# Optimization experiments

Hardware: AMD Instinct MI355X
Metric: run time of the kernel (lower is better)

## Reference

```python
import jax, jax.numpy as jnp
import numpy as np

BS, NS, NSTEP = 128, 1024, 8
IN_DIM, HID, MLP = 768, 512, 512
NEG = -100000.0


def setup_inputs() -> dict:
    key = jax.random.key(0)
    ks = jax.random.split(key, 12)
    s_h = 1.0 / np.sqrt(HID)
    s_cat = 1.0 / np.sqrt(HID + IN_DIM)
    s_m = 1.0 / np.sqrt(MLP)
    # gumbel noise implements Categorical sampling as argmax(logits + gumbel)
    u = jax.random.uniform(ks[9], (NSTEP, BS, NS), jnp.float32, 1e-7, 1.0 - 1e-7)
    return {
        "target_emb": jax.random.normal(ks[0], (BS, IN_DIM), jnp.float32),
        "ctx_emb": jax.random.normal(ks[1], (BS, NS, IN_DIM), jnp.float32),
        "target_len": jax.random.randint(ks[2], (BS,), 1, 32),
        "ctx_len": jax.random.randint(ks[3], (BS,), NSTEP, NS + 1),
        "n_step": NSTEP,
        "W_ih": jax.random.normal(ks[4], (4 * HID, IN_DIM), jnp.float32) * s_h,
        "W_hh": jax.random.normal(ks[5], (4 * HID, HID), jnp.float32) * s_h,
        "b_ih": jnp.zeros((4 * HID,), jnp.float32),
        "b_hh": jnp.zeros((4 * HID,), jnp.float32),
        "W1c": jax.random.normal(ks[6], (MLP, IN_DIM), jnp.float32) * s_cat,
        "W1h": jax.random.normal(ks[7], (MLP, HID), jnp.float32) * s_cat,
        "b1": jnp.zeros((MLP,), jnp.float32),
        "w2": jax.random.normal(ks[8], (MLP,), jnp.float32) * s_m,
        "b2": jnp.zeros((), jnp.float32),
        "gumbel": -jnp.log(-jnp.log(u)),
    }


def reference(target_emb, ctx_emb, target_len, ctx_len, n_step,
              W_ih, W_hh, b_ih, b_hh, W1c, W1h, b1, w2, b2, gumbel):
    bs, ns, in_dim = ctx_emb.shape
    hid = W_hh.shape[1]
    # mlp1 split: ctx part is constant across steps (concat([ctx, h]) @ W1^T = ctx@W1c^T + h@W1h^T)
    ctx_part = jnp.einsum('bnd,md->bnm', ctx_emb, W1c) + b1  # [bs, ns, mlp]
    mask0 = jnp.where(jnp.arange(ns)[None, :] >= ctx_len[:, None], NEG, 0.0).astype(jnp.float32)
    h0 = jnp.zeros((bs, hid), jnp.float32)
    c0 = jnp.zeros((bs, hid), jnp.float32)
    lp0 = jnp.zeros((bs,), jnp.float32)
    batch_idx = jnp.arange(bs)

    def step(carry, g):
        h, c, mask, x, lp = carry
        # LSTMCell (torch gate order: i, f, g, o); dropout is identity (eval semantics)
        gates = x @ W_ih.T + b_ih + h @ W_hh.T + b_hh
        i_g, f_g, g_g, o_g = jnp.split(gates, 4, axis=-1)
        c_new = jax.nn.sigmoid(f_g) * c + jax.nn.sigmoid(i_g) * jnp.tanh(g_g)
        h_new = jax.nn.sigmoid(o_g) * jnp.tanh(c_new)
        # attention-style MLP score
        pre = ctx_part + (h_new @ W1h.T)[:, None, :]          # [bs, ns, mlp]
        sc = jnp.tanh(pre) @ w2 + b2 + mask                   # [bs, ns]
        # Categorical(probs=softmax(sc)).sample() via Gumbel-argmax
        out = jnp.argmax(sc + g, axis=-1)                     # [bs]
        lp = lp + jnp.take_along_axis(jax.nn.log_softmax(sc, axis=-1), out[:, None], 1)[:, 0]
        mask = mask.at[batch_idx, out].set(NEG)
        x_new = jnp.take_along_axis(ctx_emb, out[:, None, None], axis=1)[:, 0, :]
        return (h_new, c_new, mask, x_new, lp), out

    (h, c, mask, x, log_probs), outputs = jax.lax.scan(
        step, (h0, c0, mask0, target_emb, lp0), gumbel)
    return outputs, log_probs
```

## Files before the change

kernel.cpp:

```cpp
#include <hip/hip_runtime.h>
#include <hip/hip_bf16.h>

#define BSZ 128
#define NSQ 1024
#define NSTEPC 8
#define IND 768
#define HIDD 512
#define G4D 2048
#define MLPD 512
#define KXD 1280
#define NEGV -100000.0f
#define KSG 16
#define KSH 8
#define MSPLIT 4

typedef __attribute__((ext_vector_type(4))) float f32x4;
typedef __attribute__((ext_vector_type(8))) short short8v;

__device__ __forceinline__ float bf2f(unsigned short u) {
  unsigned int x = ((unsigned int)u) << 16;
  return __builtin_bit_cast(float, x);
}

__device__ __forceinline__ float tanh_fast(float x) {
  x = fminf(fmaxf(x, -15.0f), 15.0f);
  float e = __builtin_amdgcn_exp2f(x * 2.8853900817779268f);
  float r = __builtin_amdgcn_rcpf(e + 1.0f);
  return fmaf(-2.0f, r, 1.0f);
}

__global__ __launch_bounds__(256) void k_init(
    const float* __restrict__ te, const int* __restrict__ cl,
    float* __restrict__ mask, float* __restrict__ xh,
    float* __restrict__ cst, float* __restrict__ lp) {
  const int b = blockIdx.x, tid = threadIdx.x;
  const int L = cl[b];
  for (int n = tid; n < NSQ; n += 256) mask[(size_t)b*NSQ + n] = (n >= L) ? NEGV : 0.0f;
  for (int d = tid; d < IND; d += 256) xh[(size_t)b*KXD + d] = te[(size_t)b*IND + d];
  for (int j = tid; j < HIDD; j += 256) {
    xh[(size_t)b*KXD + IND + j] = 0.0f;
    cst[(size_t)b*HIDD + j] = 0.0f;
  }
  if (tid == 0) lp[b] = 0.0f;
}

__global__ __launch_bounds__(256) void k_ctx_mfma(
    const float* __restrict__ A,
    const float* __restrict__ W,
    const float* __restrict__ bias,
    const int* __restrict__ clen,
    float* __restrict__ cp) {
  __shared__ short sCh[128*32], sCl[128*32], sWh[128*32], sWl[128*32];
  __shared__ float sb1[128];
  const int m0 = blockIdx.x * 128;
  const int i0 = blockIdx.y * 128;
  const int b = i0 >> 10;
  const int nbase = i0 & 1023;
  if (nbase >= clen[b]) return;
  const int tid = threadIdx.x;
  if (tid < 128) sb1[tid] = bias[m0 + tid];
  const int lane = tid & 63;
  const int wid = tid >> 6;
  const int wm = wid & 1, wn = wid >> 1;
  const int l15 = lane & 15, l4 = lane >> 4;

  f32x4 acc[4][4] = {};

  for (int k0 = 0; k0 < IND; k0 += 32) {
#pragma unroll
    for (int u = 0; u < 2; ++u) {
      const int c = tid + u * 256;
      const int row = c >> 2, kcs = c & 3;
      const int kread = kcs ^ ((row >> 1) & 3);
      const int off = row * 32 + kcs * 8;
      {
        const float* s = W + (size_t)(m0 + row) * IND + k0 + kread * 8;
        const float4 f0 = *(const float4*)s, f1 = *(const float4*)(s + 4);
        const float fv[8] = {f0.x, f0.y, f0.z, f0.w, f1.x, f1.y, f1.z, f1.w};
        short8v hi, lo;
#pragma unroll
        for (int j = 0; j < 8; ++j) {
          const unsigned int ub = __builtin_bit_cast(unsigned int, fv[j]);
          const unsigned int hb = ub & 0xFFFF0000u;
          const float lf = fv[j] - __builtin_bit_cast(float, hb);
          hi[j] = (short)(hb >> 16);
          lo[j] = (short)(__builtin_bit_cast(unsigned int, lf) >> 16);
        }
        *(short8v*)&sWh[off] = hi;
        *(short8v*)&sWl[off] = lo;
      }
      {
        const float* s = A + (size_t)(i0 + row) * IND + k0 + kread * 8;
        const float4 f0 = *(const float4*)s, f1 = *(const float4*)(s + 4);
        const float fv[8] = {f0.x, f0.y, f0.z, f0.w, f1.x, f1.y, f1.z, f1.w};
        short8v hi, lo;
#pragma unroll
        for (int j = 0; j < 8; ++j) {
          const unsigned int ub = __builtin_bit_cast(unsigned int, fv[j]);
          const unsigned int hb = ub & 0xFFFF0000u;
          const float lf = fv[j] - __builtin_bit_cast(float, hb);
          hi[j] = (short)(hb >> 16);
          lo[j] = (short)(__builtin_bit_cast(unsigned int, lf) >> 16);
        }
        *(short8v*)&sCh[off] = hi;
        *(short8v*)&sCl[off] = lo;
      }
    }
    __syncthreads();
    short8v wh[4], wl[4], chv[4], clv[4];
#pragma unroll
    for (int f = 0; f < 4; ++f) {
      const int rw = wm * 64 + f * 16 + l15;
      const int offw = rw * 32 + ((l4 ^ ((rw >> 1) & 3)) << 3);
      wh[f] = *(const short8v*)&sWh[offw];
      wl[f] = *(const short8v*)&sWl[offw];
      const int rc = wn * 64 + f * 16 + l15;
      const int offc = rc * 32 + ((l4 ^ ((rc >> 1) & 3)) << 3);
      chv[f] = *(const short8v*)&sCh[offc];
      clv[f] = *(const short8v*)&sCl[offc];
    }
#pragma unroll
    for (int fm = 0; fm < 4; ++fm)
#pragma unroll
      for (int fn = 0; fn < 4; ++fn) {
        acc[fm][fn] = __builtin_amdgcn_mfma_f32_16x16x32_bf16(wh[fm], chv[fn], acc[fm][fn], 0, 0, 0);
        acc[fm][fn] = __builtin_amdgcn_mfma_f32_16x16x32_bf16(wh[fm], clv[fn], acc[fm][fn], 0, 0, 0);
        acc[fm][fn] = __builtin_amdgcn_mfma_f32_16x16x32_bf16(wl[fm], chv[fn], acc[fm][fn], 0, 0, 0);
      }
    __syncthreads();
  }
#pragma unroll
  for (int fm = 0; fm < 4; ++fm) {
#pragma unroll
    for (int r = 0; r < 4; ++r) {
      const int m = m0 + wm * 64 + fm * 16 + l4 * 4 + r;
      const float bb = sb1[m - m0];
      float* dst = cp + (((size_t)(b * MLPD + m)) << 10) + nbase + wn * 64 + l15;
#pragma unroll
      for (int fn = 0; fn < 4; ++fn)
        dst[fn * 16] = acc[fm][fn][r] + bb;
    }
  }
}

__global__ __launch_bounds__(256) void k_pgemm(
    const float* __restrict__ A, int lda, int acol,
    const float* __restrict__ B0, int ldb0, int kb,
    const float* __restrict__ B1, int ldb1,
    int kTiles, int N, float* __restrict__ P) {
  __shared__ float As[16][128];
  __shared__ float Bs[16][132];
  const int n0 = blockIdx.x * 128;
  const int kc0 = blockIdx.y * kTiles * 16;
  const int tid = threadIdx.x;
  const int tn = tid & 15;
  const int ta = tid >> 4;
  float acc[8][8] = {};
  for (int t = 0; t < kTiles; ++t) {
    const int k0 = kc0 + t * 16;
#pragma unroll
    for (int u = 0; u < 2; ++u) {
      const int v = tid + u * 256;
      const int r = v >> 2, kc = v & 3;
      const float4 a4 = *(const float4*)(A + (size_t)r * lda + acol + k0 + kc * 4);
      As[kc*4+0][r] = a4.x; As[kc*4+1][r] = a4.y; As[kc*4+2][r] = a4.z; As[kc*4+3][r] = a4.w;
      const float* bp = (k0 < kb) ? (B0 + (size_t)(n0 + r) * ldb0 + k0 + kc * 4)
                                  : (B1 + (size_t)(n0 + r) * ldb1 + (k0 - kb) + kc * 4);
      const float4 b4 = *(const float4*)bp;
      Bs[kc*4+0][r] = b4.x; Bs[kc*4+1][r] = b4.y; Bs[kc*4+2][r] = b4.z; Bs[kc*4+3][r] = b4.w;
    }
    __syncthreads();
#pragma unroll
    for (int kk = 0; kk < 16; ++kk) {
      float av[8], bv[8];
#pragma unroll
      for (int q = 0; q < 8; ++q) av[q] = As[kk][ta*8+q];
#pragma unroll
      for (int q = 0; q < 8; ++q) bv[q] = Bs[kk][tn*8+q];
#pragma unroll
      for (int ri = 0; ri < 8; ++ri)
#pragma unroll
        for (int ni = 0; ni < 8; ++ni)
          acc[ri][ni] = fmaf(av[ri], bv[ni], acc[ri][ni]);
    }
    __syncthreads();
  }
#pragma unroll
  for (int ri = 0; ri < 8; ++ri) {
    const int i = ta * 8 + ri;
    float* p = P + ((size_t)blockIdx.y * BSZ + i) * N + n0 + tn * 8;
    *(float4*)(p + 0) = make_float4(acc[ri][0], acc[ri][1], acc[ri][2], acc[ri][3]);
    *(float4*)(p + 4) = make_float4(acc[ri][4], acc[ri][5], acc[ri][6], acc[ri][7]);
  }
}

__global__ __launch_bounds__(512) void k_lstm(
    const float* __restrict__ gp, const float* __restrict__ b_ih,
    const float* __restrict__ b_hh, float* __restrict__ cst, float* __restrict__ xh) {
  const int b = blockIdx.x, j = threadIdx.x;
  float g[4];
#pragma unroll
  for (int q = 0; q < 4; ++q) {
    float s = b_ih[q*HIDD + j] + b_hh[q*HIDD + j];
#pragma unroll
    for (int ks = 0; ks < KSG; ++ks) s += gp[((size_t)ks*BSZ + b)*G4D + q*HIDD + j];
    g[q] = s;
  }
  const float c_old = cst[(size_t)b*HIDD + j];
  const float ig = 1.0f / (1.0f + expf(-g[0]));
  const float fg = 1.0f / (1.0f + expf(-g[1]));
  const float gg = tanhf(g[2]);
  const float og = 1.0f / (1.0f + expf(-g[3]));
  const float cn = fg * c_old + ig * gg;
  const float hn = og * tanhf(cn);
  cst[(size_t)b*HIDD + j] = cn;
  xh[(size_t)b*KXD + IND + j] = hn;
}

__global__ __launch_bounds__(256) void k_scores(
    const float* __restrict__ cp, const float* __restrict__ hpp,
    const float* __restrict__ w2, const int* __restrict__ clen,
    float* __restrict__ psc) {
  const int mh = blockIdx.x;
  const int b = blockIdx.y;
  const int tid = threadIdx.x;
  __shared__ float hs[128], ws[128];
  if (tid < 128) {
    const int m = mh * 128 + tid;
    float s = 0.0f;
#pragma unroll
    for (int ks = 0; ks < KSH; ++ks) s += hpp[((size_t)ks*BSZ + b)*MLPD + m];
    hs[tid] = s;
    ws[tid] = w2[m];
  }
  __syncthreads();
  const int len = clen[b];
  const int n0 = tid * 4;
  if (n0 >= len) return;
  float ax = 0, ay = 0, az = 0, aw = 0;
  const float* base = cp + ((size_t)b * MLPD + mh * 128) * NSQ + n0;
#pragma unroll 4
  for (int mm = 0; mm < 128; ++mm) {
    const float4 c4 = *(const float4*)(base + (size_t)mm * NSQ);
    const float h = hs[mm], w = ws[mm];
    ax = fmaf(tanh_fast(c4.x + h), w, ax);
    ay = fmaf(tanh_fast(c4.y + h), w, ay);
    az = fmaf(tanh_fast(c4.z + h), w, az);
    aw = fmaf(tanh_fast(c4.w + h), w, aw);
  }
  *(float4*)(psc + ((size_t)b * MSPLIT + mh) * NSQ + n0) = make_float4(ax, ay, az, aw);
}

__global__ __launch_bounds__(256) void k_argmax(
    const float* __restrict__ psc, float* __restrict__ mask,
    const float* __restrict__ gum, const float* __restrict__ b2p,
    float* __restrict__ lp, const float* __restrict__ ctx,
    float* __restrict__ xh, float* __restrict__ outv, int step) {
  const int b = blockIdx.x, tid = threadIdx.x;
  __shared__ float rv[256], rs[256], rm[256];
  __shared__ int ri[256];
  __shared__ int sel;
  const float b2 = b2p[0];
  const int n0 = tid * 4;
  const float4 m4 = *(const float4*)(mask + (size_t)b * NSQ + n0);
  float sc[4] = {b2 + m4.x, b2 + m4.y, b2 + m4.z, b2 + m4.w};
#pragma unroll
  for (int mh = 0; mh < MSPLIT; ++mh) {
    const float4 p4 = *(const float4*)(psc + ((size_t)b * MSPLIT + mh) * NSQ + n0);
    sc[0] += p4.x; sc[1] += p4.y; sc[2] += p4.z; sc[3] += p4.w;
  }
  const float4 g4 = *(const float4*)(gum + ((size_t)step * BSZ + b) * NSQ + n0);
  const float gv[4] = {g4.x, g4.y, g4.z, g4.w};
  float bestv = -1e30f, bests = 0.0f, msc = -1e30f;
  int bestn = 0;
#pragma unroll
  for (int q = 0; q < 4; ++q) {
    const float v = sc[q] + gv[q];
    if (v > bestv) { bestv = v; bestn = n0 + q; bests = sc[q]; }
    msc = fmaxf(msc, sc[q]);
  }
  rv[tid] = bestv; ri[tid] = bestn; rs[tid] = bests; rm[tid] = msc;
  __syncthreads();
  for (int o = 128; o > 0; o >>= 1) {
    if (tid < o) {
      if (rv[tid+o] > rv[tid] || (rv[tid+o] == rv[tid] && ri[tid+o] < ri[tid])) {
        rv[tid] = rv[tid+o]; ri[tid] = ri[tid+o]; rs[tid] = rs[tid+o];
      }
      rm[tid] = fmaxf(rm[tid], rm[tid+o]);
    }
    __syncthreads();
  }
  const float M = rm[0];
  __syncthreads();
  float se = 0.0f;
#pragma unroll
  for (int q = 0; q < 4; ++q)
    se += __builtin_amdgcn_exp2f((sc[q] - M) * 1.4426950408889634f);
  rm[tid] = se;
  __syncthreads();
  for (int o = 128; o > 0; o >>= 1) {
    if (tid < o) rm[tid] += rm[tid+o];
    __syncthreads();
  }
  if (tid == 0) {
    const int n = ri[0];
    const float lse = M + logf(rm[0]);
    const float nlp = lp[b] + rs[0] - lse;
    lp[b] = nlp;
    mask[(size_t)b * NSQ + n] = NEGV;
    outv[step * BSZ + b] = (float)n;
    if (step == NSTEPC - 1) outv[NSTEPC * BSZ + b] = nlp;
    sel = n;
  }
  __syncthreads();
  const int n = sel;
  const float4* src = (const float4*)(ctx + ((size_t)b * NSQ + n) * IND);
  float4* dst = (float4*)(xh + (size_t)b * KXD);
  for (int d = tid; d < IND / 4; d += 256) dst[d] = src[d];
}

extern "C" void kernel_launch(void* const* d_in, const int* in_sizes, int n_in,
                              void* d_out, int out_size, void* d_ws, size_t ws_size,
                              hipStream_t stream) {
  const float* target_emb = (const float*)d_in[0];
  const float* ctx_emb   = (const float*)d_in[1];
  const int*   ctx_len   = (const int*)d_in[3];
  const float* W_ih = (const float*)d_in[5];
  const float* W_hh = (const float*)d_in[6];
  const float* b_ih = (const float*)d_in[7];
  const float* b_hh = (const float*)d_in[8];
  const float* W1c  = (const float*)d_in[9];
  const float* W1h  = (const float*)d_in[10];
  const float* b1   = (const float*)d_in[11];
  const float* w2   = (const float*)d_in[12];
  const float* b2   = (const float*)d_in[13];
  const float* gumbel = (const float*)d_in[14];
  float* out = (float*)d_out;

  float* ws = (float*)d_ws;
  size_t off = 0;
  auto alloc = [&](size_t n) { float* p = ws + off; off += (n + 63) & ~(size_t)63; return p; };

  float* cp   = alloc((size_t)BSZ * MLPD * NSQ);
  float* gp   = alloc((size_t)KSG * BSZ * G4D);
  float* hpp  = alloc((size_t)KSH * BSZ * MLPD);
  float* psc  = alloc((size_t)BSZ * MSPLIT * NSQ);
  float* mask = alloc((size_t)BSZ * NSQ);
  float* xh   = alloc((size_t)BSZ * KXD);
  float* cst  = alloc((size_t)BSZ * HIDD);
  float* lp   = alloc(128);

  k_init<<<BSZ, 256, 0, stream>>>(target_emb, ctx_len, mask, xh, cst, lp);

  k_ctx_mfma<<<dim3(MLPD/128, (BSZ*NSQ)/128), 256, 0, stream>>>(
      ctx_emb, W1c, b1, ctx_len, cp);

  for (int t = 0; t < NSTEPC; ++t) {
    k_pgemm<<<dim3(G4D/128, KSG), 256, 0, stream>>>(
        xh, KXD, 0, W_ih, IND, IND, W_hh, HIDD, 5, G4D, gp);
    k_lstm<<<BSZ, 512, 0, stream>>>(gp, b_ih, b_hh, cst, xh);
    k_pgemm<<<dim3(MLPD/128, KSH), 256, 0, stream>>>(
        xh, KXD, IND, W1h, HIDD, 1 << 30, nullptr, 0, 4, MLPD, hpp);
    k_scores<<<dim3(MSPLIT, BSZ), 256, 0, stream>>>(cp, hpp, w2, ctx_len, psc);
    k_argmax<<<BSZ, 256, 0, stream>>>(psc, mask, gumbel, b2, lp, ctx_emb, xh, out, t);
  }
}
```

Measured before the change: 909.2 us.

## Pre-split W1c to bf16 hi/lo and double-buffer the ctx GEMM with async LDS loads

Adds a prep kernel that splits W1c once into swizzled bf16 hi/lo tiles, so the context GEMM no longer re-splits the weight in every block. The new ctx kernel streams the weight tiles directly into LDS with global_load_lds and double-buffers both operands, prefetching the next K tile while the MFMAs run on the current one. Block indices are remapped so that blocks sharing ctx rows run close together, which should improve cache reuse. In exchange it adds an extra launch, extra workspace, and a larger LDS footprint from the doubled buffers, which may lower occupancy.

Result: faster. 857.7 us (-5.7%).

```diff
diff --git a/kernel.cpp b/kernel.cpp
--- a/kernel.cpp
+++ b/kernel.cpp
@@ -17,9 +17,22 @@
 typedef __attribute__((ext_vector_type(4))) float f32x4;
 typedef __attribute__((ext_vector_type(8))) short short8v;
 
-__device__ __forceinline__ float bf2f(unsigned short u) {
-  unsigned int x = ((unsigned int)u) << 16;
-  return __builtin_bit_cast(float, x);
+__device__ __forceinline__ void gl16(const unsigned short* g, unsigned short* l) {
+  __builtin_amdgcn_global_load_lds(
+      (const __attribute__((address_space(1))) unsigned int*)(g),
+      (__attribute__((address_space(3))) unsigned int*)(l), 16, 0, 0);
+}
+
+__device__ __forceinline__ void split2(float4 f0, float4 f1, short8v& hi, short8v& lo) {
+  float fv[8] = {f0.x, f0.y, f0.z, f0.w, f1.x, f1.y, f1.z, f1.w};
+#pragma unroll
+  for (int j = 0; j < 8; ++j) {
+    const unsigned ub = __builtin_bit_cast(unsigned, fv[j]);
+    const unsigned hb = ub & 0xFFFF0000u;
+    const float lf = fv[j] - __builtin_bit_cast(float, hb);
+    hi[j] = (short)(hb >> 16);
+    lo[j] = (short)(__builtin_bit_cast(unsigned, lf) >> 16);
+  }
 }
 
 __device__ __forceinline__ float tanh_fast(float x) {
@@ -27,6 +40,23 @@
   float e = __builtin_amdgcn_exp2f(x * 2.8853900817779268f);
   float r = __builtin_amdgcn_rcpf(e + 1.0f);
   return fmaf(-2.0f, r, 1.0f);
+}
+
+__global__ __launch_bounds__(256) void k_prep_w1c(
+    const float* __restrict__ W1c,
+    unsigned short* __restrict__ wch, unsigned short* __restrict__ wcl) {
+  const int c = blockIdx.x * 256 + threadIdx.x;
+  if (c >= 49152) return;
+  const int row = c / 96, wc = c - row * 96;
+  const int tile = wc >> 2, c4 = wc & 3;
+  const int slot = c4 ^ ((row >> 1) & 3);
+  const size_t unit = ((size_t)((row >> 7) * 24 + tile) * 128 + (row & 127)) * 4 + slot;
+  const float* src = W1c + (size_t)row * IND + wc * 8;
+  const float4 f0 = *(const float4*)src, f1 = *(const float4*)(src + 4);
+  short8v hi, lo;
+  split2(f0, f1, hi, lo);
+  *(short8v*)(wch + unit * 8) = hi;
+  *(short8v*)(wcl + unit * 8) = lo;
 }
 
 __global__ __launch_bounds__(256) void k_init(
@@ -44,89 +74,99 @@
   if (tid == 0) lp[b] = 0.0f;
 }
 
-__global__ __launch_bounds__(256) void k_ctx_mfma(
-    const float* __restrict__ A,
-    const float* __restrict__ W,
-    const float* __restrict__ bias,
-    const int* __restrict__ clen,
+__global__ __launch_bounds__(256) void k_ctx5(
+    const float* __restrict__ ctx,
+    const unsigned short* __restrict__ wch, const unsigned short* __restrict__ wcl,
+    const float* __restrict__ bias, const int* __restrict__ clen,
     float* __restrict__ cp) {
-  __shared__ short sCh[128*32], sCl[128*32], sWh[128*32], sWl[128*32];
-  __shared__ float sb1[128];
-  const int m0 = blockIdx.x * 128;
-  const int i0 = blockIdx.y * 128;
-  const int b = i0 >> 10;
-  const int nbase = i0 & 1023;
+  __shared__ __align__(16) unsigned short sWh[2][4096], sWl[2][4096];
+  __shared__ __align__(16) unsigned short sCh[2][4096], sCl[2][4096];
+  const int bid = blockIdx.x;
+  const int v = ((bid & 7) << 9) + (bid >> 3);
+  const int mx = v & 3;
+  const int rbC = v >> 2;
+  const int b = rbC >> 3;
+  const int nbase = (rbC & 7) << 7;
   if (nbase >= clen[b]) return;
+  const int i0 = rbC << 7;
+  const int m0 = mx << 7;
   const int tid = threadIdx.x;
-  if (tid < 128) sb1[tid] = bias[m0 + tid];
-  const int lane = tid & 63;
-  const int wid = tid >> 6;
+  const int lane = tid & 63, wid = tid >> 6;
   const int wm = wid & 1, wn = wid >> 1;
   const int l15 = lane & 15, l4 = lane >> 4;
+  const int c0r = tid >> 2, cs = tid & 3;
+  const int c1r = 64 + c0r;
+  const int k0rd = cs ^ ((c0r >> 1) & 3);
+  const int k1rd = cs ^ ((c1r >> 1) & 3);
+  const float* csrc0 = ctx + (size_t)(i0 + c0r) * IND + k0rd * 8;
+  const float* csrc1 = ctx + (size_t)(i0 + c1r) * IND + k1rd * 8;
+
+#pragma unroll
+  for (int i = 0; i < 4; ++i) {
+    const int seg = wid * 4 + i;
+    const unsigned short* g = ((seg & 8) ? wcl : wch) +
+        (size_t)(mx * 24) * 4096 + (seg & 7) * 512 + lane * 8;
+    unsigned short* l = ((seg & 8) ? sWl[0] : sWh[0]) + (seg & 7) * 512;
+    gl16(g, l);
+  }
+  {
+    short8v hi, lo;
+    split2(*(const float4*)csrc0, *(const float4*)(csrc0 + 4), hi, lo);
+    *(short8v*)&sCh[0][tid * 8] = hi;
+    *(short8v*)&sCl[0][tid * 8] = lo;
+    split2(*(const float4*)csrc1, *(const float4*)(csrc1 + 4), hi, lo);
+    *(short8v*)&sCh[0][(256 + tid) * 8] = hi;
+    *(short8v*)&sCl[0][(256 + tid) * 8] = lo;
+  }
+  __syncthreads();
 
   f32x4 acc[4][4] = {};
-
-  for (int k0 = 0; k0 < IND; k0 += 32) {
-#pragma unroll
-    for (int u = 0; u < 2; ++u) {
-      const int c = tid + u * 256;
-      const int row = c >> 2, kcs = c & 3;
-      const int kread = kcs ^ ((row >> 1) & 3);
-      const int off = row * 32 + kcs * 8;
-      {
-        const float* s = W + (size_t)(m0 + row) * IND + k0 + kread * 8;
-        const float4 f0 = *(const float4*)s, f1 = *(const float4*)(s + 4);
-        const float fv[8] = {f0.x, f0.y, f0.z, f0.w, f1.x, f1.y, f1.z, f1.w};
-        short8v hi, lo;
-#pragma unroll
-        for (int j = 0; j < 8; ++j) {
-          const unsigned int ub = __builtin_bit_cast(unsigned int, fv[j]);
-          const unsigned int hb = ub & 0xFFFF0000u;
-          const float lf = fv[j] - __builtin_bit_cast(float, hb);
-          hi[j] = (short)(hb >> 16);
-          lo[j] = (short)(__builtin_bit_cast(unsigned int, lf) >> 16);
-        }
-        *(short8v*)&sWh[off] = hi;
-        *(short8v*)&sWl[off] = lo;
+  for (int t = 0; t < 24; ++t) {
+    const int cur = t & 1, nb = cur ^ 1;
+    float4 r00, r01, r10, r11;
+    if (t + 1 < 24) {
+#pragma unroll
+      for (int i = 0; i < 4; ++i) {
+        const int seg = wid * 4 + i;
+        const unsigned short* g = ((seg & 8) ? wcl : wch) +
+            (size_t)(mx * 24 + t + 1) * 4096 + (seg & 7) * 512 + lane * 8;
+        unsigned short* l = ((seg & 8) ? sWl[nb] : sWh[nb]) + (seg & 7) * 512;
+        gl16(g, l);
       }
-      {
-        const float* s = A + (size_t)(i0 + row) * IND + k0 + kread * 8;
-        const float4 f0 = *(const float4*)s, f1 = *(const float4*)(s + 4);
-        const float fv[8] = {f0.x, f0.y, f0.z, f0.w, f1.x, f1.y, f1.z, f1.w};
-        short8v hi, lo;
-#pragma unroll
-        for (int j = 0; j < 8; ++j) {
-          const unsigned int ub = __builtin_bit_cast(unsigned int, fv[j]);
-          const unsigned int hb = ub & 0xFFFF0000u;
-          const float lf = fv[j] - __builtin_bit_cast(float, hb);
-          hi[j] = (short)(hb >> 16);
-          lo[j] = (short)(__builtin_bit_cast(unsigned int, lf) >> 16);
-        }
-        *(short8v*)&sCh[off] = hi;
-        *(short8v*)&sCl[off] = lo;
-      }
-    }
-    __syncthreads();
-    short8v wh[4], wl[4], chv[4], clv[4];
+      r00 = *(const float4*)(csrc0 + (t + 1) * 32);
+      r01 = *(const float4*)(csrc0 + (t + 1) * 32 + 4);
+      r10 = *(const float4*)(csrc1 + (t + 1) * 32);
+      r11 = *(const float4*)(csrc1 + (t + 1) * 32 + 4);
+    }
+    short8v ah[4], al[4], bh[4], bl[4];
 #pragma unroll
     for (int f = 0; f < 4; ++f) {
       const int rw = wm * 64 + f * 16 + l15;
-      const int offw = rw * 32 + ((l4 ^ ((rw >> 1) & 3)) << 3);
-      wh[f] = *(const short8v*)&sWh[offw];
-      wl[f] = *(const short8v*)&sWl[offw];
+      const int so = (l4 ^ ((rw >> 1) & 3)) << 3;
+      ah[f] = *(const short8v*)&sWh[cur][rw * 32 + so];
+      al[f] = *(const short8v*)&sWl[cur][rw * 32 + so];
       const int rc = wn * 64 + f * 16 + l15;
-      const int offc = rc * 32 + ((l4 ^ ((rc >> 1) & 3)) << 3);
-      chv[f] = *(const short8v*)&sCh[offc];
-      clv[f] = *(const short8v*)&sCl[offc];
+      const int sc = (l4 ^ ((rc >> 1) & 3)) << 3;
+      bh[f] = *(const short8v*)&sCh[cur][rc * 32 + sc];
+      bl[f] = *(const short8v*)&sCl[cur][rc * 32 + sc];
     }
 #pragma unroll
     for (int fm = 0; fm < 4; ++fm)
 #pragma unroll
       for (int fn = 0; fn < 4; ++fn) {
-        acc[fm][fn] = __builtin_amdgcn_mfma_f32_16x16x32_bf16(wh[fm], chv[fn], acc[fm][fn], 0, 0, 0);
-        acc[fm][fn] = __builtin_amdgcn_mfma_f32_16x16x32_bf16(wh[fm], clv[fn], acc[fm][fn], 0, 0, 0);
-        acc[fm][fn] = __builtin_amdgcn_mfma_f32_16x16x32_bf16(wl[fm], chv[fn], acc[fm][fn], 0, 0, 0);
+        acc[fm][fn] = __builtin_amdgcn_mfma_f32_16x16x32_bf16(ah[fm], bh[fn], acc[fm][fn], 0, 0, 0);
+        acc[fm][fn] = __builtin_amdgcn_mfma_f32_16x16x32_bf16(ah[fm], bl[fn], acc[fm][fn], 0, 0, 0);
+        acc[fm][fn] = __builtin_amdgcn_mfma_f32_16x16x32_bf16(al[fm], bh[fn], acc[fm][fn], 0, 0, 0);
       }
+    if (t + 1 < 24) {
+      short8v hi, lo;
+      split2(r00, r01, hi, lo);
+      *(short8v*)&sCh[nb][tid * 8] = hi;
+      *(short8v*)&sCl[nb][tid * 8] = lo;
+      split2(r10, r11, hi, lo);
+      *(short8v*)&sCh[nb][(256 + tid) * 8] = hi;
+      *(short8v*)&sCl[nb][(256 + tid) * 8] = lo;
+    }
     __syncthreads();
   }
 #pragma unroll
@@ -134,7 +174,7 @@
 #pragma unroll
     for (int r = 0; r < 4; ++r) {
       const int m = m0 + wm * 64 + fm * 16 + l4 * 4 + r;
-      const float bb = sb1[m - m0];
+      const float bb = bias[m];
       float* dst = cp + (((size_t)(b * MLPD + m)) << 10) + nbase + wn * 64 + l15;
 #pragma unroll
       for (int fn = 0; fn < 4; ++fn)
@@ -349,11 +389,12 @@
   float* xh   = alloc((size_t)BSZ * KXD);
   float* cst  = alloc((size_t)BSZ * HIDD);
   float* lp   = alloc(128);
-
+  unsigned short* wch = (unsigned short*)alloc(196608);
+  unsigned short* wcl = (unsigned short*)alloc(196608);
+
+  k_prep_w1c<<<192, 256, 0, stream>>>(W1c, wch, wcl);
   k_init<<<BSZ, 256, 0, stream>>>(target_emb, ctx_len, mask, xh, cst, lp);
-
-  k_ctx_mfma<<<dim3(MLPD/128, (BSZ*NSQ)/128), 256, 0, stream>>>(
-      ctx_emb, W1c, b1, ctx_len, cp);
+  k_ctx5<<<4096, 256, 0, stream>>>(ctx_emb, wch, wcl, b1, ctx_len, cp);
 
   for (int t = 0; t < NSTEPC; ++t) {
     k_pgemm<<<dim3(G4D/128, KSG), 256, 0, stream>>>(
```
